# Optimization experiments

Hardware: AMD Instinct MI355X
Metric: run time of the kernel (lower is better)

## Reference

```python
import jax, jax.numpy as jnp
import numpy as np
from jax.scipy.special import logsumexp

B, N = 256, 65536
NEG_INF = jnp.float32(-1e30)  # acts as -inf for logsumexp, keeps grads finite


def setup_inputs() -> dict:
    key = jax.random.key(0)
    k1, k2 = jax.random.split(key)
    sim = jax.random.uniform(k1, (B, N), dtype=jnp.float32)
    label = jax.random.uniform(k2, (B, N), dtype=jnp.float32)
    return {"sim": sim, "label": label}


def _ranking_loss(sim, label):
    m = 0.2
    gamma = 64.0
    delta_p = 1.0 - m  # 0.8
    delta_n = m        # 0.2

    pos_mask = label > 0.5
    neg_mask = label < 0.25

    # ---- positives: logit_p = -relu(0.8 - sim).detach() * (sim - 0.8) * gamma ----
    alpha_p = jax.lax.stop_gradient(jnp.maximum(0.8 - sim, 0.0))
    logit_p = -alpha_p * (sim - delta_p) * gamma
    lse_p = logsumexp(jnp.where(pos_mask, logit_p, NEG_INF), axis=1)
    # torch fallback: no positives -> logit_p = [0.0], logsumexp == 0
    lse_p = jnp.where(pos_mask.any(axis=1), lse_p, 0.0)

    # ---- negatives: if >20 negatives, keep only top-10 largest sims ----
    alpha_n_all = jax.lax.stop_gradient(jnp.maximum(sim - 0.2, 0.0))
    logit_n_all = alpha_n_all * (sim - delta_n) * gamma
    lse_n_all = logsumexp(jnp.where(neg_mask, logit_n_all, NEG_INF), axis=1)

    neg_sim_masked = jnp.where(neg_mask, sim, NEG_INF)
    top_v, _ = jax.lax.top_k(neg_sim_masked, 10)  # [B, 10]
    alpha_n_top = jax.lax.stop_gradient(jnp.maximum(top_v - 0.2, 0.0))
    logit_n_top = alpha_n_top * (top_v - delta_n) * gamma
    lse_n_top = logsumexp(logit_n_top, axis=1)

    n_neg = neg_mask.sum(axis=1)
    lse_n = jnp.where(n_neg > 20, lse_n_top, lse_n_all)

    loss_loc = jax.nn.softplus(lse_n + lse_p).sum()
    return loss_loc / sim.shape[0]  # reduction='mean'


def reference(sim, label):
    return _ranking_loss(sim, label)
```

## Files before the change

kernel.cpp:

```cpp
#include <hip/hip_runtime.h>
#include <cmath>

#define NEG_INF (-1.0e30f)

static constexpr int B = 256;
static constexpr int N = 65536;
static constexpr int CHUNKS = 4;
static constexpr int THREADS = 512;
static constexpr int NBLOCKS = B * CHUNKS;
static constexpr int CHUNK_ELEMS = N / CHUNKS;
static constexpr int ITER = CHUNK_ELEMS / 4 / THREADS;
static constexpr float C_OFF = 40.96f;
static constexpr float CAND_THRESH = 0.98f;
static constexpr int CAP = 1024;
static constexpr int PSTRIDE = 16;

__device__ __forceinline__ float wave_sum_f(float v) {
#pragma unroll
  for (int off = 32; off >= 1; off >>= 1) v += __shfl_xor(v, off, 64);
  return v;
}
__device__ __forceinline__ int wave_sum_i(int v) {
#pragma unroll
  for (int off = 32; off >= 1; off >>= 1) v += __shfl_xor(v, off, 64);
  return v;
}

__device__ __forceinline__ void insert10(float t[16], float s) {
  if (s > t[9]) {
    t[9] = s;
#pragma unroll
    for (int i = 9; i > 0; --i) {
      float a = t[i - 1], b = t[i];
      t[i - 1] = fmaxf(a, b);
      t[i] = fminf(a, b);
    }
  }
}

__device__ __forceinline__ void merge_lists_shfl(float t[16], int off) {
  float b[16];
#pragma unroll
  for (int i = 0; i < 16; ++i) b[i] = __shfl_xor(t[i], off, 64);
  float c[16];
#pragma unroll
  for (int i = 0; i < 16; ++i) c[i] = fmaxf(t[i], b[15 - i]);
#pragma unroll
  for (int s = 8; s >= 1; s >>= 1) {
#pragma unroll
    for (int i = 0; i < 16; ++i) {
      if ((i & s) == 0) {
        float lo = c[i], hi = c[i + s];
        c[i] = fmaxf(lo, hi);
        c[i + s] = fminf(lo, hi);
      }
    }
  }
#pragma unroll
  for (int i = 0; i < 16; ++i) t[i] = c[i];
}

__device__ __forceinline__ void proc(float s, float l, float& s_p, float& s_n,
                                     int& nn, float* cand, int* cnt) {
  const bool pos = l > 0.5f;
  const bool neg = l < 0.25f;
  float d = pos ? (0.8f - s) : (s - 0.2f);
  float r = fmaxf(d, 0.f);
  float e = __expf(fmaf(64.f * r, r, -C_OFF));
  if (pos) s_p += e;
  if (neg) {
    s_n += e;
    ++nn;
    if (s > CAND_THRESH) {
      int p = atomicAdd(cnt, 1);
      if (p < CAP) cand[p] = s;
    }
  }
}

__global__ void __launch_bounds__(THREADS, 8) ranking_partial_kernel(
    const float* __restrict__ sim, const float* __restrict__ label,
    float* __restrict__ partials) {
  const int blk = blockIdx.x;
  const int row = blk >> 2;
  const int chunk = blk & 3;
  const int tid = threadIdx.x;
  const int wave = tid >> 6, lane = tid & 63;

  __shared__ float cand[CAP];
  __shared__ int cnt;
  __shared__ float ls_p[8], ls_n[8];
  __shared__ int ls_c[8];
  __shared__ float ltop[8][16];
  if (tid == 0) cnt = 0;
  __syncthreads();

  const size_t base4 =
      (size_t)row * (N / 4) + (size_t)chunk * (CHUNK_ELEMS / 4);
  const float4* sim4 = reinterpret_cast<const float4*>(sim) + base4;
  const float4* lab4 = reinterpret_cast<const float4*>(label) + base4;

  float s_p = 0.f, s_n = 0.f;
  int nn = 0;

#pragma unroll 2
  for (int it = 0; it < ITER; ++it) {
    float4 sv = sim4[it * THREADS + tid];
    float4 lv = lab4[it * THREADS + tid];
    proc(sv.x, lv.x, s_p, s_n, nn, cand, &cnt);
    proc(sv.y, lv.y, s_p, s_n, nn, cand, &cnt);
    proc(sv.z, lv.z, s_p, s_n, nn, cand, &cnt);
    proc(sv.w, lv.w, s_p, s_n, nn, cand, &cnt);
  }

  s_p = wave_sum_f(s_p);
  s_n = wave_sum_f(s_n);
  nn = wave_sum_i(nn);
  if (lane == 0) {
    ls_p[wave] = s_p;
    ls_n[wave] = s_n;
    ls_c[wave] = nn;
  }
  __syncthreads();

  float sp_tot = 0.f, sn_tot = 0.f;
  int nn_tot = 0;
#pragma unroll
  for (int i = 0; i < 8; ++i) {
    sp_tot += ls_p[i];
    sn_tot += ls_n[i];
    nn_tot += ls_c[i];
  }
  const int cnt_tot = cnt;
  const bool bad = (cnt_tot > CAP) || (cnt_tot < 10 && cnt_tot < nn_tot);

  float t[16];
#pragma unroll
  for (int i = 0; i < 16; ++i) t[i] = NEG_INF;

  float* P = partials + (size_t)blk * PSTRIDE;

  if (!bad) {
    if (wave == 0) {
      const int c = cnt_tot < CAP ? cnt_tot : CAP;
      for (int i = lane; i < c; i += 64) insert10(t, cand[i]);
#pragma unroll
      for (int off = 1; off < 64; off <<= 1) merge_lists_shfl(t, off);
      if (lane == 0) {
        P[0] = sp_tot;
        P[1] = sn_tot;
        P[2] = (float)nn_tot;
        P[3] = 0.f;
#pragma unroll
        for (int i = 0; i < 10; ++i) P[4 + i] = t[i];
      }
    }
  } else {
    for (int it = 0; it < ITER; ++it) {
      float4 sv = sim4[it * THREADS + tid];
      float4 lv = lab4[it * THREADS + tid];
      if (lv.x < 0.25f) insert10(t, sv.x);
      if (lv.y < 0.25f) insert10(t, sv.y);
      if (lv.z < 0.25f) insert10(t, sv.z);
      if (lv.w < 0.25f) insert10(t, sv.w);
    }
#pragma unroll
    for (int off = 1; off < 64; off <<= 1) merge_lists_shfl(t, off);
    if (lane == 0) {
#pragma unroll
      for (int i = 0; i < 16; ++i) ltop[wave][i] = t[i];
    }
    __syncthreads();
    if (wave == 0) {
      float m[16];
      if (lane < 8) {
#pragma unroll
        for (int i = 0; i < 16; ++i) m[i] = ltop[lane][i];
      } else {
#pragma unroll
        for (int i = 0; i < 16; ++i) m[i] = NEG_INF;
      }
      merge_lists_shfl(m, 1);
      merge_lists_shfl(m, 2);
      merge_lists_shfl(m, 4);
      if (lane == 0) {
        P[0] = sp_tot;
        P[1] = sn_tot;
        P[2] = (float)nn_tot;
        P[3] = 0.f;
#pragma unroll
        for (int i = 0; i < 10; ++i) P[4 + i] = m[i];
      }
    }
  }
}

__global__ void __launch_bounds__(256) final_kernel(
    const float* __restrict__ partials, float* __restrict__ out) {
  const int r = threadIdx.x;
  float sp = 0.f, sn = 0.f, nnf = 0.f;
  float t[16];
#pragma unroll
  for (int i = 0; i < 16; ++i) t[i] = NEG_INF;
#pragma unroll
  for (int c = 0; c < CHUNKS; ++c) {
    const float* P = partials + (size_t)(r * CHUNKS + c) * PSTRIDE;
    sp += P[0];
    sn += P[1];
    nnf += P[2];
#pragma unroll
    for (int i = 0; i < 10; ++i) insert10(t, P[4 + i]);
  }

  float lse_p = (sp > 0.f) ? (C_OFF + __logf(sp)) : 0.f;
  float lse_n_all = (sn > 0.f) ? (C_OFF + __logf(sn)) : NEG_INF;

  float mx = NEG_INF;
  float lg[10];
#pragma unroll
  for (int i = 0; i < 10; ++i) {
    float v = t[i];
    float a = fmaxf(v - 0.2f, 0.f);
    float lo = a * (v - 0.2f) * 64.f;
    lg[i] = lo;
    mx = fmaxf(mx, lo);
  }
  float ss = 0.f;
#pragma unroll
  for (int i = 0; i < 10; ++i) ss += __expf(lg[i] - mx);
  float lse_n_top = mx + __logf(ss);

  float lse_n = (nnf > 20.5f) ? lse_n_top : lse_n_all;
  float x = lse_n + lse_p;
  float loss = fmaxf(x, 0.f) + log1pf(__expf(-fabsf(x)));

  loss = wave_sum_f(loss);
  __shared__ float ws[4];
  if ((r & 63) == 0) ws[r >> 6] = loss;
  __syncthreads();
  if (r == 0) out[0] = (ws[0] + ws[1] + ws[2] + ws[3]) * (1.0f / 256.0f);
}

extern "C" void kernel_launch(void* const* d_in, const int* in_sizes, int n_in,
                              void* d_out, int out_size, void* d_ws, size_t ws_size,
                              hipStream_t stream) {
  const float* sim = (const float*)d_in[0];
  const float* label = (const float*)d_in[1];
  float* out = (float*)d_out;
  float* partials = (float*)d_ws;
  ranking_partial_kernel<<<dim3(NBLOCKS), dim3(THREADS), 0, stream>>>(sim, label, partials);
  final_kernel<<<dim3(1), dim3(256), 0, stream>>>(partials, out);
}
```

Baseline: 156.1 us.

## Preload chunk into registers, keep per-thread top-4 candidates, shrink blocks

Splits each row into 8 chunks of 256-thread blocks, and loads a thread's whole chunk into registers up front so all global loads are in flight together. Per-element shared-memory atomics for top-k candidates are replaced by a per-thread register top-4 list that is flushed once. The fallback path reuses the register copy instead of re-reading global memory. This raises register pressure (16 float4 per thread) and adds a fallback trigger when any thread sees more than four candidates.

Result: slower. 159.4 us (+2.1%).

```diff
diff --git a/kernel.cpp b/kernel.cpp
--- a/kernel.cpp
+++ b/kernel.cpp
@@ -5,14 +5,14 @@
 
 static constexpr int B = 256;
 static constexpr int N = 65536;
-static constexpr int CHUNKS = 4;
-static constexpr int THREADS = 512;
+static constexpr int CHUNKS = 8;
+static constexpr int THREADS = 256;
 static constexpr int NBLOCKS = B * CHUNKS;
 static constexpr int CHUNK_ELEMS = N / CHUNKS;
 static constexpr int ITER = CHUNK_ELEMS / 4 / THREADS;
 static constexpr float C_OFF = 40.96f;
 static constexpr float CAND_THRESH = 0.98f;
-static constexpr int CAP = 1024;
+static constexpr int CAP = 512;
 static constexpr int PSTRIDE = 16;
 
 __device__ __forceinline__ float wave_sum_f(float v) {
@@ -23,6 +23,11 @@
 __device__ __forceinline__ int wave_sum_i(int v) {
 #pragma unroll
   for (int off = 32; off >= 1; off >>= 1) v += __shfl_xor(v, off, 64);
+  return v;
+}
+__device__ __forceinline__ int wave_max_i(int v) {
+#pragma unroll
+  for (int off = 32; off >= 1; off >>= 1) v = max(v, __shfl_xor(v, off, 64));
   return v;
 }
 
@@ -61,78 +66,96 @@
 }
 
 __device__ __forceinline__ void proc(float s, float l, float& s_p, float& s_n,
-                                     int& nn, float* cand, int* cnt) {
+                                     int& nn, int& cc, float c4[4]) {
   const bool pos = l > 0.5f;
   const bool neg = l < 0.25f;
   float d = pos ? (0.8f - s) : (s - 0.2f);
   float r = fmaxf(d, 0.f);
   float e = __expf(fmaf(64.f * r, r, -C_OFF));
-  if (pos) s_p += e;
-  if (neg) {
-    s_n += e;
-    ++nn;
-    if (s > CAND_THRESH) {
-      int p = atomicAdd(cnt, 1);
-      if (p < CAP) cand[p] = s;
-    }
-  }
-}
-
-__global__ void __launch_bounds__(THREADS, 8) ranking_partial_kernel(
+  s_p += pos ? e : 0.f;
+  s_n += neg ? e : 0.f;
+  nn += neg ? 1 : 0;
+  if (neg && s > CAND_THRESH) {
+    ++cc;
+    if (s > c4[3]) {
+      c4[3] = s;
+#pragma unroll
+      for (int i = 3; i > 0; --i) {
+        float a = c4[i - 1], b = c4[i];
+        c4[i - 1] = fmaxf(a, b);
+        c4[i] = fminf(a, b);
+      }
+    }
+  }
+}
+
+__global__ void __launch_bounds__(THREADS) ranking_partial_kernel(
     const float* __restrict__ sim, const float* __restrict__ label,
     float* __restrict__ partials) {
   const int blk = blockIdx.x;
-  const int row = blk >> 2;
-  const int chunk = blk & 3;
+  const int row = blk >> 3;
+  const int chunk = blk & 7;
   const int tid = threadIdx.x;
   const int wave = tid >> 6, lane = tid & 63;
 
   __shared__ float cand[CAP];
   __shared__ int cnt;
-  __shared__ float ls_p[8], ls_n[8];
-  __shared__ int ls_c[8];
-  __shared__ float ltop[8][16];
+  __shared__ float ls_p[4], ls_n[4];
+  __shared__ int ls_c[4], ls_cc[4], ls_ccmax[4];
+  __shared__ float ltop[4][16];
   if (tid == 0) cnt = 0;
   __syncthreads();
 
-  const size_t base4 =
-      (size_t)row * (N / 4) + (size_t)chunk * (CHUNK_ELEMS / 4);
+  const size_t base4 = (size_t)row * (N / 4) + (size_t)chunk * (CHUNK_ELEMS / 4);
   const float4* sim4 = reinterpret_cast<const float4*>(sim) + base4;
   const float4* lab4 = reinterpret_cast<const float4*>(label) + base4;
 
+  float4 S[ITER], L[ITER];
+#pragma unroll
+  for (int it = 0; it < ITER; ++it) {
+    S[it] = sim4[it * THREADS + tid];
+    L[it] = lab4[it * THREADS + tid];
+  }
+
   float s_p = 0.f, s_n = 0.f;
-  int nn = 0;
-
-#pragma unroll 2
+  int nn = 0, cc = 0;
+  float c4[4] = {NEG_INF, NEG_INF, NEG_INF, NEG_INF};
+
+#pragma unroll
   for (int it = 0; it < ITER; ++it) {
-    float4 sv = sim4[it * THREADS + tid];
-    float4 lv = lab4[it * THREADS + tid];
-    proc(sv.x, lv.x, s_p, s_n, nn, cand, &cnt);
-    proc(sv.y, lv.y, s_p, s_n, nn, cand, &cnt);
-    proc(sv.z, lv.z, s_p, s_n, nn, cand, &cnt);
-    proc(sv.w, lv.w, s_p, s_n, nn, cand, &cnt);
-  }
-
-  s_p = wave_sum_f(s_p);
-  s_n = wave_sum_f(s_n);
-  nn = wave_sum_i(nn);
+    proc(S[it].x, L[it].x, s_p, s_n, nn, cc, c4);
+    proc(S[it].y, L[it].y, s_p, s_n, nn, cc, c4);
+    proc(S[it].z, L[it].z, s_p, s_n, nn, cc, c4);
+    proc(S[it].w, L[it].w, s_p, s_n, nn, cc, c4);
+  }
+
+  const int nst = min(cc, 4);
+  for (int i = 0; i < nst; ++i) {
+    int p = atomicAdd(&cnt, 1);
+    if (p < CAP) cand[p] = c4[i];
+  }
+
+  float sw_p = wave_sum_f(s_p);
+  float sw_n = wave_sum_f(s_n);
+  int nw = wave_sum_i(nn);
+  int ccw = wave_sum_i(cc);
+  int ccmx = wave_max_i(cc);
   if (lane == 0) {
-    ls_p[wave] = s_p;
-    ls_n[wave] = s_n;
-    ls_c[wave] = nn;
+    ls_p[wave] = sw_p;
+    ls_n[wave] = sw_n;
+    ls_c[wave] = nw;
+    ls_cc[wave] = ccw;
+    ls_ccmax[wave] = ccmx;
   }
   __syncthreads();
 
-  float sp_tot = 0.f, sn_tot = 0.f;
-  int nn_tot = 0;
-#pragma unroll
-  for (int i = 0; i < 8; ++i) {
-    sp_tot += ls_p[i];
-    sn_tot += ls_n[i];
-    nn_tot += ls_c[i];
-  }
-  const int cnt_tot = cnt;
-  const bool bad = (cnt_tot > CAP) || (cnt_tot < 10 && cnt_tot < nn_tot);
+  float sp_tot = ls_p[0] + ls_p[1] + ls_p[2] + ls_p[3];
+  float sn_tot = ls_n[0] + ls_n[1] + ls_n[2] + ls_n[3];
+  const int nn_tot = ls_c[0] + ls_c[1] + ls_c[2] + ls_c[3];
+  const int cc_tot = ls_cc[0] + ls_cc[1] + ls_cc[2] + ls_cc[3];
+  const int cc_max = max(max(ls_ccmax[0], ls_ccmax[1]), max(ls_ccmax[2], ls_ccmax[3]));
+
+  const bool bad = (cc_max > 4) || (cc_tot > CAP) || (cc_tot < 10 && cc_tot < nn_tot);
 
   float t[16];
 #pragma unroll
@@ -142,7 +165,7 @@
 
   if (!bad) {
     if (wave == 0) {
-      const int c = cnt_tot < CAP ? cnt_tot : CAP;
+      const int c = cnt < CAP ? cnt : CAP;
       for (int i = lane; i < c; i += 64) insert10(t, cand[i]);
 #pragma unroll
       for (int off = 1; off < 64; off <<= 1) merge_lists_shfl(t, off);
@@ -156,13 +179,12 @@
       }
     }
   } else {
+#pragma unroll
     for (int it = 0; it < ITER; ++it) {
-      float4 sv = sim4[it * THREADS + tid];
-      float4 lv = lab4[it * THREADS + tid];
-      if (lv.x < 0.25f) insert10(t, sv.x);
-      if (lv.y < 0.25f) insert10(t, sv.y);
-      if (lv.z < 0.25f) insert10(t, sv.z);
-      if (lv.w < 0.25f) insert10(t, sv.w);
+      if (L[it].x < 0.25f) insert10(t, S[it].x);
+      if (L[it].y < 0.25f) insert10(t, S[it].y);
+      if (L[it].z < 0.25f) insert10(t, S[it].z);
+      if (L[it].w < 0.25f) insert10(t, S[it].w);
     }
 #pragma unroll
     for (int off = 1; off < 64; off <<= 1) merge_lists_shfl(t, off);
@@ -173,7 +195,7 @@
     __syncthreads();
     if (wave == 0) {
       float m[16];
-      if (lane < 8) {
+      if (lane < 4) {
 #pragma unroll
         for (int i = 0; i < 16; ++i) m[i] = ltop[lane][i];
       } else {
@@ -182,7 +204,6 @@
       }
       merge_lists_shfl(m, 1);
       merge_lists_shfl(m, 2);
-      merge_lists_shfl(m, 4);
       if (lane == 0) {
         P[0] = sp_tot;
         P[1] = sn_tot;
```
